# Kernel tuning notes

Measured on AMD Instinct MI355X. Metric: run time of the kernel, lower is better.

Reference implementation:

```python
import jax, jax.numpy as jnp
import numpy as np
import math

B = 8192
D_MODEL = 1
D_STATE = 16
D_CONV = 4
EXPAND = 2
NSLICES = 4
NFEAT = 256
NTRIP = 100
D_INNER = EXPAND * D_MODEL
DT_RANK = math.ceil(D_MODEL / 16)
EPS = 1e-5


def setup_inputs():
    key = jax.random.key(0)
    ks = iter(jax.random.split(key, 64))
    def rn(shape, s=0.1):
        return jax.random.normal(next(ks), shape, dtype=jnp.float32) * s
    dt_bias0 = jnp.float32(math.log(math.expm1(0.01)))  # standard mamba dt init
    A_init = jnp.log(jnp.tile(jnp.arange(1, D_STATE + 1, dtype=jnp.float32), (D_INNER, 1)))
    inp = {}
    inp['x'] = jax.random.normal(next(ks), (B, NFEAT), dtype=jnp.float32)
    inp['norm_w'] = jnp.ones((D_MODEL,), jnp.float32)
    inp['norm_b'] = rn((D_MODEL,), 0.1)
    inp['in_proj_w'] = rn((2 * D_INNER, D_MODEL), 0.5)
    for d in ('f', 'b', 's'):
        inp['conv_w_' + d] = rn((D_INNER, D_CONV), 0.5)
        inp['conv_b_' + d] = rn((D_INNER,), 0.1)
        inp['xproj_w_' + d] = rn((DT_RANK + 2 * D_STATE, D_INNER), 0.3)
        inp['dtproj_w_' + d] = rn((D_INNER, DT_RANK), 0.3)
        inp['dtproj_b_' + d] = rn((D_INNER,), 0.05) + dt_bias0
        inp['A_log_' + d] = A_init + rn((D_INNER, D_STATE), 0.01)
        inp['Dskip_' + d] = jnp.ones((D_INNER,), jnp.float32) + rn((D_INNER,), 0.01)
    inp['out_proj_w'] = rn((D_MODEL, D_INNER), 0.3)
    inp['w1'] = rn((512, NFEAT), 0.05); inp['b1'] = rn((512,), 0.05)
    inp['w2'] = rn((256, 512), 0.05); inp['b2'] = rn((256,), 0.05)
    inp['w3'] = rn((NTRIP, 256), 0.05); inp['b3'] = rn((NTRIP,), 0.05)
    return inp


def _mamba_dir(xz, conv_w, conv_b, xproj_w, dtproj_w, dtproj_b, A_log, Dskip):
    # xz: [b, 2*d_inner, l] -> y: [b, d_inner, l]; one causal selective scan.
    b, _, l = xz.shape
    x, z = jnp.split(xz, 2, axis=1)
    x = jax.lax.conv_general_dilated(
        x, conv_w[:, None, :], (1,), [(D_CONV - 1, 0)],
        dimension_numbers=('NCH', 'OIH', 'NCH'), feature_group_count=D_INNER)
    x = jax.nn.silu(x + conv_b[None, :, None])               # [b, d, l]
    xdbl = jnp.einsum('bdl,kd->bkl', x, xproj_w)             # [b, r+2n, l]
    delta = jax.nn.softplus(
        jnp.einsum('brl,dr->bdl', xdbl[:, :DT_RANK], dtproj_w) + dtproj_b[None, :, None])
    Bs = xdbl[:, DT_RANK:DT_RANK + D_STATE]                  # [b, n, l]
    Cs = xdbl[:, DT_RANK + D_STATE:]                         # [b, n, l]
    A = -jnp.exp(A_log)                                      # [d, n]

    def step(h, inp):
        dlt, u, Bt, Ct = inp                                 # [b,d],[b,d],[b,n],[b,n]
        h = jnp.exp(dlt[..., None] * A) * h + (dlt * u)[..., None] * Bt[:, None, :]
        return h, jnp.einsum('bdn,bn->bd', h, Ct)

    h0 = jnp.zeros((b, D_INNER, D_STATE), x.dtype)
    _, ys = jax.lax.scan(step, h0, (delta.transpose(2, 0, 1), x.transpose(2, 0, 1),
                                    Bs.transpose(2, 0, 1), Cs.transpose(2, 0, 1)))
    y = ys.transpose(1, 2, 0) + x * Dskip[None, :, None]
    return y * jax.nn.silu(z)


def reference(x, norm_w, norm_b, in_proj_w,
              conv_w_f, conv_b_f, xproj_w_f, dtproj_w_f, dtproj_b_f, A_log_f, Dskip_f,
              conv_w_b, conv_b_b, xproj_w_b, dtproj_w_b, dtproj_b_b, A_log_b, Dskip_b,
              conv_w_s, conv_b_s, xproj_w_s, dtproj_w_s, dtproj_b_s, A_log_s, Dskip_s,
              out_proj_w, w1, b1, w2, b2, w3, b3):
    h = x[:, :, None]                                        # [B, L, 1]
    mu = h.mean(-1, keepdims=True)
    var = ((h - mu) ** 2).mean(-1, keepdims=True)
    hn = (h - mu) / jnp.sqrt(var + EPS) * norm_w + norm_b    # LayerNorm over dim=1
    xz = jnp.einsum('bld,ed->bel', hn, in_proj_w)            # [B, 2*d_inner, L]
    b, c, l = xz.shape
    out_f = _mamba_dir(xz, conv_w_f, conv_b_f, xproj_w_f, dtproj_w_f, dtproj_b_f, A_log_f, Dskip_f)
    out_b = jnp.flip(_mamba_dir(jnp.flip(xz, -1), conv_w_b, conv_b_b, xproj_w_b,
                                dtproj_w_b, dtproj_b_b, A_log_b, Dskip_b), -1)
    # slice interleave: chunk(nslices, -1) -> stack(-1) -> flatten(-2)
    xz_s = xz.reshape(b, c, NSLICES, l // NSLICES).transpose(0, 1, 3, 2).reshape(b, c, l)
    out_s = _mamba_dir(xz_s, conv_w_s, conv_b_s, xproj_w_s, dtproj_w_s, dtproj_b_s, A_log_s, Dskip_s)
    out_s = out_s.reshape(b, D_INNER, NSLICES, l // NSLICES).transpose(0, 1, 3, 2).reshape(b, D_INNER, l)
    y = jnp.einsum('bdl,ed->ble', out_f + out_b + out_s, out_proj_w)  # [B, L, 1]
    y = y[:, :, 0]                                           # transpose(-1,-2).squeeze(1)
    h1 = jax.nn.elu(y @ w1.T + b1)
    h2 = jax.nn.elu(h1 @ w2.T + b2)
    return h2 @ w3.T + b3
```

## Files before the change

kernel.cpp:

```cpp
#include <hip/hip_runtime.h>
#include <math.h>

#define SEQL 256

struct PK {
    const float* norm_b;
    const float* in_proj_w;
    const float* conv_w[3];
    const float* conv_b[3];
    const float* xproj_w[3];
    const float* dtproj_w[3];
    const float* dtproj_b[3];
    const float* A_log[3];
    const float* Dskip[3];
    const float* out_proj_w;
    const float* w1; const float* b1;
    float* h1;
};

__device__ __forceinline__ float silu_f(float x)     { return x / (1.0f + expf(-x)); }
__device__ __forceinline__ float softplus_f(float x) { return x > 0.f ? x + log1pf(expf(-x)) : log1pf(expf(x)); }
__device__ __forceinline__ float elu_f(float x)      { return x > 0.f ? x : expm1f(x); }

__global__ __launch_bounds__(64) void k_scan_mlp1(PK p) {
    __shared__ float xs_c[3][4][2];
    __shared__ float dl_c[3][4][2];
    __shared__ float hc[SEQL][49];
    __shared__ __align__(16) float yrow[SEQL];

    const int tid = threadIdx.x;
    const float nb0 = p.norm_b[0];
    const float c0  = nb0 * p.in_proj_w[0];
    const float c1  = nb0 * p.in_proj_w[1];

    if (tid < 12) {
        const int dir = tid >> 2, cls = tid & 3;
        const float* cw  = p.conv_w[dir];
        const float* cb  = p.conv_b[dir];
        const float* xp  = p.xproj_w[dir];
        const float* dtw = p.dtproj_w[dir];
        const float* dtb = p.dtproj_b[dir];
        float xsv[2];
        for (int d = 0; d < 2; ++d) {
            float s = 0.f;
            for (int k = 3 - cls; k < 4; ++k) s += cw[d * 4 + k];
            xsv[d] = silu_f((d == 0 ? c0 : c1) * s + cb[d]);
            xs_c[dir][cls][d] = xsv[d];
        }
        const float xd0 = xp[0] * xsv[0] + xp[1] * xsv[1];
        dl_c[dir][cls][0] = softplus_f(dtw[0] * xd0 + dtb[0]);
        dl_c[dir][cls][1] = softplus_f(dtw[1] * xd0 + dtb[1]);
    }
    __syncthreads();

    if (tid < 48) {
        const int dir = tid / 16;
        const int r   = tid % 16;
        const int d   = r / 8;
        const int k   = r % 8;
        const int n0  = 2 * k, n1 = 2 * k + 1;
        const float* xp = p.xproj_w[dir];
        const float A0 = -expf(p.A_log[dir][d * 16 + n0]);
        const float A1 = -expf(p.A_log[dir][d * 16 + n1]);
        const float b00 = xp[(1 + n0) * 2],  b01 = xp[(1 + n0) * 2 + 1];
        const float b10 = xp[(1 + n1) * 2],  b11 = xp[(1 + n1) * 2 + 1];
        const float c00 = xp[(17 + n0) * 2], c01 = xp[(17 + n0) * 2 + 1];
        const float c10 = xp[(17 + n1) * 2], c11 = xp[(17 + n1) * 2 + 1];
        const int q = (dir * 2 + d) * 8 + k;

        float e0[4], f0[4], e1[4], f1[4], cp0[4], cp1[4];
        #pragma unroll
        for (int cls = 0; cls < 4; ++cls) {
            const float x0 = xs_c[dir][cls][0], x1 = xs_c[dir][cls][1];
            const float dlt = dl_c[dir][cls][d];
            const float u   = (d == 0) ? x0 : x1;
            const float du  = dlt * u;
            e0[cls] = expf(dlt * A0);  f0[cls] = du * (b00 * x0 + b01 * x1);
            e1[cls] = expf(dlt * A1);  f1[cls] = du * (b10 * x0 + b11 * x1);
            cp0[cls] = c00 * x0 + c01 * x1;
            cp1[cls] = c10 * x0 + c11 * x1;
        }
        float h0 = 0.f, h1v = 0.f;
        #pragma unroll
        for (int l = 0; l < 3; ++l) {
            h0  = e0[l] * h0  + f0[l];
            h1v = e1[l] * h1v + f1[l];
            hc[l][q] = h0 * cp0[l] + h1v * cp1[l];
        }
        const float E0 = e0[3], F0 = f0[3], E1 = e1[3], F1 = f1[3];
        const float P0 = cp0[3], P1 = cp1[3];
        for (int l = 3; l < SEQL; ++l) {
            h0  = E0 * h0  + F0;
            h1v = E1 * h1v + F1;
            hc[l][q] = h0 * P0 + h1v * P1;
        }
    }
    __syncthreads();

    {
        const float opw0 = p.out_proj_w[0], opw1 = p.out_proj_w[1];
        const float sz0  = silu_f(nb0 * p.in_proj_w[2]);
        const float sz1  = silu_f(nb0 * p.in_proj_w[3]);
        for (int i = 0; i < 4; ++i) {
            const int t = i * 64 + tid;
            float acc = 0.f;
            for (int dir = 0; dir < 3; ++dir) {
                int lv;
                if      (dir == 0) lv = t;
                else if (dir == 1) lv = SEQL - 1 - t;
                else               lv = ((t & 3) << 6) + (t >> 2);
                const int cls = lv < 3 ? lv : 3;
                float s0 = 0.f, s1 = 0.f;
                for (int k = 0; k < 8; ++k) {
                    s0 += hc[lv][dir * 16 + k];
                    s1 += hc[lv][dir * 16 + 8 + k];
                }
                const float y0 = (s0 + xs_c[dir][cls][0] * p.Dskip[dir][0]) * sz0;
                const float y1 = (s1 + xs_c[dir][cls][1] * p.Dskip[dir][1]) * sz1;
                acc += opw0 * y0 + opw1 * y1;
            }
            yrow[t] = acc;
        }
    }
    __syncthreads();

    {
        const int j = blockIdx.x;
        const float4 w = reinterpret_cast<const float4*>(p.w1)[j * 64 + tid];
        const float4 y = reinterpret_cast<const float4*>(yrow)[tid];
        float s = w.x * y.x + w.y * y.y + w.z * y.z + w.w * y.w;
        for (int m = 1; m < 64; m <<= 1) s += __shfl_xor(s, m);
        if (tid == 0) p.h1[j] = elu_f(s + p.b1[j]);
    }
}

__global__ __launch_bounds__(64) void k_mlp2(const float* __restrict__ w2, const float* __restrict__ b2,
                                             const float* __restrict__ h1, float* __restrict__ h2) {
    const int j = blockIdx.x, t = threadIdx.x;
    const float4* wr = reinterpret_cast<const float4*>(w2 + j * 512);
    const float4* hv = reinterpret_cast<const float4*>(h1);
    const float4 a = wr[t],      x = hv[t];
    const float4 b = wr[t + 64], y = hv[t + 64];
    float s = a.x * x.x + a.y * x.y + a.z * x.z + a.w * x.w
            + b.x * y.x + b.y * y.y + b.z * y.z + b.w * y.w;
    for (int m = 1; m < 64; m <<= 1) s += __shfl_xor(s, m);
    if (t == 0) h2[j] = elu_f(s + b2[j]);
}

__global__ __launch_bounds__(256) void k_mlp3_bcast(const float* __restrict__ w3, const float* __restrict__ b3,
                                                    const float* __restrict__ h2, float4* __restrict__ out4) {
    __shared__ __align__(16) float h2L[256];
    __shared__ __align__(16) float rowL[100];
    const int t = threadIdx.x;
    if (t < 64) reinterpret_cast<float4*>(h2L)[t] = reinterpret_cast<const float4*>(h2)[t];
    __syncthreads();
    const int wave = t >> 6, lane = t & 63;
    for (int jj = 0; jj < 25; ++jj) {
        const int j = wave * 25 + jj;
        const float4 w = reinterpret_cast<const float4*>(w3)[j * 64 + lane];
        const float4 h = reinterpret_cast<const float4*>(h2L)[lane];
        float s = w.x * h.x + w.y * h.y + w.z * h.z + w.w * h.w;
        for (int m = 1; m < 64; m <<= 1) s += __shfl_xor(s, m);
        if (lane == 0) rowL[j] = s + b3[j];
    }
    __syncthreads();
    const float4* rowL4 = reinterpret_cast<const float4*>(rowL);
    const int base = blockIdx.x * 1024;
    #pragma unroll
    for (int i = 0; i < 4; ++i) {
        const int idx = base + i * 256 + t;
        out4[idx] = rowL4[idx % 25];
    }
}

extern "C" void kernel_launch(void* const* d_in, const int* in_sizes, int n_in,
                              void* d_out, int out_size, void* d_ws, size_t ws_size,
                              hipStream_t stream) {
    const float* const* in = (const float* const*)d_in;
    PK p;
    p.norm_b    = in[2];
    p.in_proj_w = in[3];
    for (int dir = 0; dir < 3; ++dir) {
        const int base = 4 + dir * 7;
        p.conv_w[dir]   = in[base + 0];
        p.conv_b[dir]   = in[base + 1];
        p.xproj_w[dir]  = in[base + 2];
        p.dtproj_w[dir] = in[base + 3];
        p.dtproj_b[dir] = in[base + 4];
        p.A_log[dir]    = in[base + 5];
        p.Dskip[dir]    = in[base + 6];
    }
    p.out_proj_w = in[25];
    p.w1 = in[26]; p.b1 = in[27];
    const float* w2 = in[28]; const float* b2 = in[29];
    const float* w3 = in[30]; const float* b3 = in[31];

    float* ws = (float*)d_ws;
    float* h1 = ws;
    float* h2 = ws + 512;
    p.h1 = h1;

    k_scan_mlp1<<<512, 64, 0, stream>>>(p);
    k_mlp2     <<<256, 64, 0, stream>>>(w2, b2, h1, h2);
    k_mlp3_bcast<<<200, 256, 0, stream>>>(w3, b3, h2, (float4*)d_out);
}
```

Baseline: 148.6 us.

## Fuse scan, MLP layers and broadcast into one cooperative kernel with grid syncs

Merges the three separate kernels (scan plus first MLP layer, second layer, third layer plus output broadcast) into one cooperative kernel of 512 blocks. Grid-wide barriers replace the kernel boundaries between stages, and the final broadcast is spread across all 512 blocks. The aim is to remove two launch overheads and the idle gaps between launches. In exchange it pays for three grid.sync barriers, requires all 512 blocks to be co-resident, and leaves most blocks idle during the small layer-2 and layer-3 stages.

```diff
diff --git a/kernel.cpp b/kernel.cpp
--- a/kernel.cpp
+++ b/kernel.cpp
@@ -1,9 +1,12 @@
 #include <hip/hip_runtime.h>
+#include <hip/hip_cooperative_groups.h>
 #include <math.h>
 
+namespace cg = cooperative_groups;
+
 #define SEQL 256
 
-struct PK {
+struct PC {
     const float* norm_b;
     const float* in_proj_w;
     const float* conv_w[3];
@@ -15,20 +18,29 @@
     const float* Dskip[3];
     const float* out_proj_w;
     const float* w1; const float* b1;
+    const float* w2; const float* b2;
+    const float* w3; const float* b3;
     float* h1;
+    float* h2;
+    float* row;
+    float4* out4;
 };
 
 __device__ __forceinline__ float silu_f(float x)     { return x / (1.0f + expf(-x)); }
 __device__ __forceinline__ float softplus_f(float x) { return x > 0.f ? x + log1pf(expf(-x)) : log1pf(expf(x)); }
 __device__ __forceinline__ float elu_f(float x)      { return x > 0.f ? x : expm1f(x); }
 
-__global__ __launch_bounds__(64) void k_scan_mlp1(PK p) {
+__global__ __launch_bounds__(64) void k_coop(PC p) {
+    cg::grid_group grid = cg::this_grid();
+
     __shared__ float xs_c[3][4][2];
     __shared__ float dl_c[3][4][2];
     __shared__ float hc[SEQL][49];
     __shared__ __align__(16) float yrow[SEQL];
+    __shared__ __align__(16) float rowL[100];
 
     const int tid = threadIdx.x;
+    const int bid = blockIdx.x;
     const float nb0 = p.norm_b[0];
     const float c0  = nb0 * p.in_proj_w[0];
     const float c1  = nb0 * p.in_proj_w[1];
@@ -125,51 +137,49 @@
     __syncthreads();
 
     {
-        const int j = blockIdx.x;
-        const float4 w = reinterpret_cast<const float4*>(p.w1)[j * 64 + tid];
+        const float4 w = reinterpret_cast<const float4*>(p.w1)[bid * 64 + tid];
         const float4 y = reinterpret_cast<const float4*>(yrow)[tid];
         float s = w.x * y.x + w.y * y.y + w.z * y.z + w.w * y.w;
         for (int m = 1; m < 64; m <<= 1) s += __shfl_xor(s, m);
-        if (tid == 0) p.h1[j] = elu_f(s + p.b1[j]);
-    }
-}
-
-__global__ __launch_bounds__(64) void k_mlp2(const float* __restrict__ w2, const float* __restrict__ b2,
-                                             const float* __restrict__ h1, float* __restrict__ h2) {
-    const int j = blockIdx.x, t = threadIdx.x;
-    const float4* wr = reinterpret_cast<const float4*>(w2 + j * 512);
-    const float4* hv = reinterpret_cast<const float4*>(h1);
-    const float4 a = wr[t],      x = hv[t];
-    const float4 b = wr[t + 64], y = hv[t + 64];
-    float s = a.x * x.x + a.y * x.y + a.z * x.z + a.w * x.w
-            + b.x * y.x + b.y * y.y + b.z * y.z + b.w * y.w;
-    for (int m = 1; m < 64; m <<= 1) s += __shfl_xor(s, m);
-    if (t == 0) h2[j] = elu_f(s + b2[j]);
-}
-
-__global__ __launch_bounds__(256) void k_mlp3_bcast(const float* __restrict__ w3, const float* __restrict__ b3,
-                                                    const float* __restrict__ h2, float4* __restrict__ out4) {
-    __shared__ __align__(16) float h2L[256];
-    __shared__ __align__(16) float rowL[100];
-    const int t = threadIdx.x;
-    if (t < 64) reinterpret_cast<float4*>(h2L)[t] = reinterpret_cast<const float4*>(h2)[t];
-    __syncthreads();
-    const int wave = t >> 6, lane = t & 63;
-    for (int jj = 0; jj < 25; ++jj) {
-        const int j = wave * 25 + jj;
-        const float4 w = reinterpret_cast<const float4*>(w3)[j * 64 + lane];
-        const float4 h = reinterpret_cast<const float4*>(h2L)[lane];
+        if (tid == 0) p.h1[bid] = elu_f(s + p.b1[bid]);
+    }
+    grid.sync();
+
+    if (bid < 256) {
+        const float4* wr = reinterpret_cast<const float4*>(p.w2 + bid * 512);
+        const float4* hv = reinterpret_cast<const float4*>(p.h1);
+        const float4 a = wr[tid],      x = hv[tid];
+        const float4 b = wr[tid + 64], y = hv[tid + 64];
+        float s = a.x * x.x + a.y * x.y + a.z * x.z + a.w * x.w
+                + b.x * y.x + b.y * y.y + b.z * y.z + b.w * y.w;
+        for (int m = 1; m < 64; m <<= 1) s += __shfl_xor(s, m);
+        if (tid == 0) p.h2[bid] = elu_f(s + p.b2[bid]);
+    }
+    grid.sync();
+
+    if (bid < 100) {
+        const float4 w = reinterpret_cast<const float4*>(p.w3 + bid * 256)[tid];
+        const float4 h = reinterpret_cast<const float4*>(p.h2)[tid];
         float s = w.x * h.x + w.y * h.y + w.z * h.z + w.w * h.w;
         for (int m = 1; m < 64; m <<= 1) s += __shfl_xor(s, m);
-        if (lane == 0) rowL[j] = s + b3[j];
-    }
-    __syncthreads();
-    const float4* rowL4 = reinterpret_cast<const float4*>(rowL);
-    const int base = blockIdx.x * 1024;
-    #pragma unroll
-    for (int i = 0; i < 4; ++i) {
-        const int idx = base + i * 256 + t;
-        out4[idx] = rowL4[idx % 25];
+        if (tid == 0) p.row[bid] = s + p.b3[bid];
+    }
+    grid.sync();
+
+    {
+        if (tid < 25) reinterpret_cast<float4*>(rowL)[tid] =
+                          reinterpret_cast<const float4*>(p.row)[tid];
+        __syncthreads();
+        const float4* rowL4 = reinterpret_cast<const float4*>(rowL);
+        const int base = bid * 400;
+        #pragma unroll
+        for (int i = 0; i < 7; ++i) {
+            const int k = i * 64 + tid;
+            if (k < 400) {
+                const int idx = base + k;
+                p.out4[idx] = rowL4[idx % 25];
+            }
+        }
     }
 }
 
@@ -177,7 +187,7 @@
                               void* d_out, int out_size, void* d_ws, size_t ws_size,
                               hipStream_t stream) {
     const float* const* in = (const float* const*)d_in;
-    PK p;
+    PC p;
     p.norm_b    = in[2];
     p.in_proj_w = in[3];
     for (int dir = 0; dir < 3; ++dir) {
@@ -192,15 +202,15 @@
     }
     p.out_proj_w = in[25];
     p.w1 = in[26]; p.b1 = in[27];
-    const float* w2 = in[28]; const float* b2 = in[29];
-    const float* w3 = in[30]; const float* b3 = in[31];
+    p.w2 = in[28]; p.b2 = in[29];
+    p.w3 = in[30]; p.b3 = in[31];
 
     float* ws = (float*)d_ws;
-    float* h1 = ws;
-    float* h2 = ws + 512;
-    p.h1 = h1;
-
-    k_scan_mlp1<<<512, 64, 0, stream>>>(p);
-    k_mlp2     <<<256, 64, 0, stream>>>(w2, b2, h1, h2);
-    k_mlp3_bcast<<<200, 256, 0, stream>>>(w3, b3, h2, (float4*)d_out);
+    p.h1  = ws;
+    p.h2  = ws + 512;
+    p.row = ws + 768;
+    p.out4 = (float4*)d_out;
+
+    void* args[] = { &p };
+    hipLaunchCooperativeKernel((void*)k_coop, dim3(512), dim3(64), args, 0, stream);
 }
```

Result: slower. 339.6 us (+128.6%).
